# Performance work log

Hardware: AMD Instinct MI355X
Metric: run time of the kernel (lower is better)

Reference implementation:

```python
import jax, jax.numpy as jnp
import numpy as np
from jax import lax

WINDOW_SIZE = 11
SIGMA = 1.5
EPS = 1e-08
C1 = 0.01 ** 2
C2 = 0.03 ** 2


def _gaussian_window(ws, sigma):
    x = jnp.arange(ws, dtype=jnp.float32)
    g = jnp.exp(-((x - ws // 2) ** 2) / (2.0 * sigma ** 2))
    g = g / g.sum()
    w2d = jnp.outer(g, g)  # (ws, ws)
    return w2d[None, None]  # (1,1,ws,ws) OIHW depthwise kernel for C=1


def _normalize(a, b):
    # per-batch min-max normalize, matching torch code exactly
    B = a.shape[0]
    fa = a.reshape(B, -1)
    fb = b.reshape(B, -1)
    mn1 = fa.min(1).reshape(B, 1, 1, 1)
    mx1 = fa.max(1).reshape(B, 1, 1, 1)
    mn2 = fb.min(1).reshape(B, 1, 1, 1)
    mx2 = fb.max(1).reshape(B, 1, 1, 1)
    a = (a - mn1) / (mx1 - mn1 + EPS)
    b = (b - mn2) / (mx2 - mn2 + EPS)
    return a, b


def _dw_conv(x, win):
    # depthwise gaussian blur, SAME-style padding ws//2 (torch conv2d is xcorr;
    # gaussian kernel is symmetric so identical)
    C = x.shape[1]
    k = jnp.broadcast_to(win, (C, 1, WINDOW_SIZE, WINDOW_SIZE))
    pad = WINDOW_SIZE // 2
    return lax.conv_general_dilated(
        x, k, window_strides=(1, 1), padding=[(pad, pad), (pad, pad)],
        feature_group_count=C,
        dimension_numbers=('NCHW', 'OIHW', 'NCHW'))


def _ssim_mean(m1, m2, win):
    mu1 = _dw_conv(m1, win)
    mu2 = _dw_conv(m2, win)
    mu1_sq = mu1 * mu1
    mu2_sq = mu2 * mu2
    mu1_mu2 = mu1 * mu2
    sigma1 = _dw_conv(m1 * m1, win) - mu1_sq
    sigma2 = _dw_conv(m2 * m2, win) - mu2_sq
    sigma12 = _dw_conv(m1 * m2, win) - mu1_mu2
    ssim_map = ((2 * mu1_mu2 + C1) * (2 * sigma12 + C2)) / \
               ((mu1_sq + mu2_sq + C1) * (sigma1 + sigma2 + C2))
    return ssim_map.mean()


def _forward(img1, img2, mask_pos, w):
    B, C, H, W = img1.shape
    cols = mask_pos[:, None] + jnp.arange(w)  # (B, w)
    idx = cols[:, None, None, :]
    s1 = jnp.take_along_axis(img1, idx, axis=3)  # (B,C,H,w)
    s2 = jnp.take_along_axis(img2, idx, axis=3)

    # Faithful to source: normalize is called inside the per-batch loop, so
    # row b is normalized (B-b) times; zero rows stay zero (0/eps).
    def body(carry, b):
        m1, m2 = carry
        m1 = m1.at[b].set(s1[b])
        m2 = m2.at[b].set(s2[b])
        m1, m2 = _normalize(m1, m2)
        return (m1, m2), None

    init = (jnp.zeros_like(s1), jnp.zeros_like(s2))
    (m1, m2), _ = lax.scan(body, init, jnp.arange(B))
    win = _gaussian_window(WINDOW_SIZE, SIGMA)
    return _ssim_mean(m1, m2, win)


def setup_inputs() -> dict:
    key = jax.random.key(0)
    k1, k2, k3 = jax.random.split(key, 3)
    B, Cc, H, W = 8, 1, 1024, 2048
    w = 1024
    img1 = jax.random.uniform(k1, (B, Cc, H, W), dtype=jnp.float32)
    img2 = jax.random.uniform(k2, (B, Cc, H, W), dtype=jnp.float32)
    mask_pos = jax.random.randint(k3, (B,), 0, W - w, dtype=jnp.int64 if jax.config.jax_enable_x64 else jnp.int32)
    return {'img1': img1, 'img2': img2, 'mask_pos': mask_pos, 'mask_width': w}


def reference(img1, img2, mask_pos, mask_width):
    return _forward(img1, img2, mask_pos, int(mask_width))
```

## Files before the change

kernel.cpp:

```cpp
#include <hip/hip_runtime.h>

#define NB 8
#define IMH 1024
#define IMW 2048
#define WM 1024
#define RPB 32
#define CPB 256
#define RBW 272

__device__ __forceinline__ unsigned int enc_f(float f) {
    unsigned int u = __float_as_uint(f);
    return (u & 0x80000000u) ? ~u : (u | 0x80000000u);
}
__device__ __forceinline__ float dec_f(unsigned int u) {
    u = (u & 0x80000000u) ? (u & 0x7fffffffu) : ~u;
    return __uint_as_float(u);
}


__global__ void k_init(unsigned int* ws) {
    int t = threadIdx.x;
    if (t < 16) { ws[t] = 0xFFFFFFFFu; ws[16 + t] = 0u; }
    if (t == 0) *((double*)(ws + 80)) = 0.0;
}

__global__ __launch_bounds__(256) void k_minmax(const float* __restrict__ img1,
                                                const float* __restrict__ img2,
                                                const int* __restrict__ mask_pos,
                                                unsigned int* __restrict__ ws) {
    int bi = blockIdx.x >> 6;
    int img = bi >> 3, b = bi & 7;
    int chunk = blockIdx.x & 63;
    const float* base = (img ? img2 : img1)
        + (size_t)b * IMH * IMW + (size_t)(chunk * 16) * IMW + mask_pos[b];
    int tid = threadIdx.x;
    float mn = 3.4e38f, mx = -3.4e38f;
    for (int idx = tid; idx < 16 * WM; idx += 256) {
        int r = idx >> 10, c = idx & (WM - 1);
        float v = base[(size_t)r * IMW + c];
        mn = fminf(mn, v); mx = fmaxf(mx, v);
    }
    for (int off = 32; off; off >>= 1) {
        mn = fminf(mn, __shfl_down(mn, off));
        mx = fmaxf(mx, __shfl_down(mx, off));
    }
    __shared__ float smn[4], smx[4];
    int lane = tid & 63, wid = tid >> 6;
    if (lane == 0) { smn[wid] = mn; smx[wid] = mx; }
    __syncthreads();
    if (tid == 0) {
        mn = fminf(fminf(smn[0], smn[1]), fminf(smn[2], smn[3]));
        mx = fmaxf(fmaxf(smx[0], smx[1]), fmaxf(smx[2], smx[3]));
        atomicMin(&ws[img * 8 + b], enc_f(mn));
        atomicMax(&ws[16 + img * 8 + b], enc_f(mx));
    }
}

__global__ __launch_bounds__(256) void k_ssim(const float* __restrict__ img1,
                                              const float* __restrict__ img2,
                                              const int* __restrict__ mask_pos,
                                              const unsigned int* __restrict__ ws,
                                              double* __restrict__ acc_g) {
    __shared__ float rb[2][2][RBW];
    __shared__ float red[4];

    const int tid = threadIdx.x;
    const int b  = blockIdx.z;
    const int cb = blockIdx.x * CPB;
    const int r0 = blockIdx.y * RPB;
    const int mp = mask_pos[b];

    float mn1, sc1, mn2, sc2;
    {
        float mnA = dec_f(ws[b]),     mxA = dec_f(ws[16 + b]);
        float mnB = dec_f(ws[8 + b]), mxB = dec_f(ws[24 + b]);
        float rngA = mxA - mnA; float d0A = rngA + 1e-8f; double DA = (double)d0A; float MA = rngA / d0A;
        float rngB = mxB - mnB; float d0B = rngB + 1e-8f; double DB = (double)d0B; float MB = rngB / d0B;
        for (int j = 0; j < 7 - b; ++j) {
            float djA = MA + 1e-8f; DA *= (double)djA; MA = MA / djA;
            float djB = MB + 1e-8f; DB *= (double)djB; MB = MB / djB;
        }
        mn1 = mnA; sc1 = (float)(1.0 / DA);
        mn2 = mnB; sc2 = (float)(1.0 / DB);
    }
    float gw[11];
    {
        float s = 0.f;
#pragma unroll
        for (int k = 0; k < 11; ++k) {
            float x = (float)((k - 5) * (k - 5));
            gw[k] = expf(-x / 4.5f);
            s += gw[k];
        }
#pragma unroll
        for (int k = 0; k < 11; ++k) gw[k] = gw[k] / s;
    }

    const float* b1 = img1 + (size_t)b * (IMH * IMW);
    const float* b2 = img2 + (size_t)b * (IMH * IMW);

    float acc[11][5];
#pragma unroll
    for (int s = 0; s < 11; ++s)
#pragma unroll
        for (int ch = 0; ch < 5; ++ch) acc[s][ch] = 0.f;

    float local = 0.f;

    {
        int rn = r0 - 5;
        float va = 0.f, vb = 0.f, wa = 0.f, wb = 0.f;
        if ((unsigned)rn < (unsigned)IMH) {
            int mcA = cb + tid - 8;
            if ((unsigned)mcA < (unsigned)WM) {
                size_t o = (size_t)rn * IMW + (size_t)(mp + mcA);
                va = (b1[o] - mn1) * sc1; vb = (b2[o] - mn2) * sc2;
            }
            if (tid < RBW - 256) {
                int mcB = cb + 248 + tid;
                if ((unsigned)mcB < (unsigned)WM) {
                    size_t o = (size_t)rn * IMW + (size_t)(mp + mcB);
                    wa = (b1[o] - mn1) * sc1; wb = (b2[o] - mn2) * sc2;
                }
            }
        }
        rb[0][0][tid] = va; rb[0][1][tid] = vb;
        if (tid < RBW - 256) { rb[0][0][256 + tid] = wa; rb[0][1][256 + tid] = wb; }
        __syncthreads();
    }

#pragma unroll 1
    for (int g = 0; g < 4; ++g) {
#pragma unroll
        for (int p = 0; p < 11; ++p) {
            const int i = g * 11 + p;
            const int par = (g + p) & 1;

            int rn = r0 - 4 + i;
            float va = 0.f, vb = 0.f, wa = 0.f, wb = 0.f;
            if ((unsigned)rn < (unsigned)IMH) {
                int mcA = cb + tid - 8;
                if ((unsigned)mcA < (unsigned)WM) {
                    size_t o = (size_t)rn * IMW + (size_t)(mp + mcA);
                    va = (b1[o] - mn1) * sc1; vb = (b2[o] - mn2) * sc2;
                }
                if (tid < RBW - 256) {
                    int mcB = cb + 248 + tid;
                    if ((unsigned)mcB < (unsigned)WM) {
                        size_t o = (size_t)rn * IMW + (size_t)(mp + mcB);
                        wa = (b1[o] - mn1) * sc1; wb = (b2[o] - mn2) * sc2;
                    }
                }
            }

            const float* c0p = &rb[par][0][tid + 3];
            const float* c1p = &rb[par][1][tid + 3];
            float ha = 0.f, hb = 0.f, haa = 0.f, hbb = 0.f, hab = 0.f;
#pragma unroll
            for (int k = 0; k < 11; ++k) {
                float av = c0p[k], bv = c1p[k], w = gw[k];
                ha  = fmaf(w, av, ha);
                hb  = fmaf(w, bv, hb);
                haa = fmaf(w, av * av, haa);
                hbb = fmaf(w, bv * bv, hbb);
                hab = fmaf(w, av * bv, hab);
            }

#pragma unroll
            for (int s = 0; s < 11; ++s) {
                const float w = gw[(p + 10 - s) % 11];
                acc[s][0] = fmaf(w, ha,  acc[s][0]);
                acc[s][1] = fmaf(w, hb,  acc[s][1]);
                acc[s][2] = fmaf(w, haa, acc[s][2]);
                acc[s][3] = fmaf(w, hbb, acc[s][3]);
                acc[s][4] = fmaf(w, hab, acc[s][4]);
            }

            if (i >= 10 && i <= 41) {
                float mu1 = acc[p][0], mu2 = acc[p][1];
                float e11 = acc[p][2], e22 = acc[p][3], e12 = acc[p][4];
                float m11 = mu1 * mu1, m22 = mu2 * mu2, m12 = mu1 * mu2;
                float num = (2.f * m12 + 1e-4f) * (2.f * (e12 - m12) + 9e-4f);
                float den = (m11 + m22 + 1e-4f) * ((e11 - m11) + (e22 - m22) + 9e-4f);
                local += num / den;
            }
            acc[p][0] = 0.f; acc[p][1] = 0.f; acc[p][2] = 0.f;
            acc[p][3] = 0.f; acc[p][4] = 0.f;

            rb[par ^ 1][0][tid] = va; rb[par ^ 1][1][tid] = vb;
            if (tid < RBW - 256) { rb[par ^ 1][0][256 + tid] = wa; rb[par ^ 1][1][256 + tid] = wb; }
            __syncthreads();
        }
    }

    for (int off = 32; off; off >>= 1) local += __shfl_down(local, off);
    int lane = tid & 63, wid = tid >> 6;
    if (lane == 0) red[wid] = local;
    __syncthreads();
    if (tid == 0) {
        double s = (double)red[0] + (double)red[1] + (double)red[2] + (double)red[3];
        atomicAdd(acc_g, s);
    }
}

__global__ void k_final(const double* __restrict__ acc, float* __restrict__ out) {
    out[0] = (float)(acc[0] * (1.0 / 8388608.0));
}

extern "C" void kernel_launch(void* const* d_in, const int* in_sizes, int n_in,
                              void* d_out, int out_size, void* d_ws, size_t ws_size,
                              hipStream_t stream) {
    const float* img1 = (const float*)d_in[0];
    const float* img2 = (const float*)d_in[1];
    const int* mask_pos = (const int*)d_in[2];
    unsigned int* ws = (unsigned int*)d_ws;
    double* acc = (double*)(ws + 80);
    float* out = (float*)d_out;

    hipLaunchKernelGGL(k_init, dim3(1), dim3(64), 0, stream, ws);
    hipLaunchKernelGGL(k_minmax, dim3(1024), dim3(256), 0, stream, img1, img2, mask_pos, ws);
    hipLaunchKernelGGL(k_ssim, dim3(WM / CPB, IMH / RPB, NB), dim3(256), 0, stream,
                       img1, img2, mask_pos, ws, acc);
    hipLaunchKernelGGL(k_final, dim3(1), dim3(1), 0, stream, acc, out);
}
```

Measured before the change: 231.5 us.

## Vectorize minmax loads, interleave SSIM smem buffer, simplify SSIM row loads

The min/max pass now reads with aligned float4 loads and scalar head/tail handling, using twice as many blocks of 8 rows each. The SSIM kernel interleaves the two images in shared memory as float2 pairs and swaps buffers with pointers. Row loads use precomputed offsets and unconditional loads followed by selects. The vertical accumulator reset is folded into a first-write assignment, and the division uses __fdividef. The changes aim to cut memory instruction count and branching, at the cost of more index arithmetic and a slightly less exact division.

```diff
diff --git a/kernel.cpp b/kernel.cpp
--- a/kernel.cpp
+++ b/kernel.cpp
@@ -6,7 +6,6 @@
 #define WM 1024
 #define RPB 32
 #define CPB 256
-#define RBW 272
 
 __device__ __forceinline__ unsigned int enc_f(float f) {
     unsigned int u = __float_as_uint(f);
@@ -28,17 +27,32 @@
                                                 const float* __restrict__ img2,
                                                 const int* __restrict__ mask_pos,
                                                 unsigned int* __restrict__ ws) {
-    int bi = blockIdx.x >> 6;
+    int bi = blockIdx.x >> 7;
     int img = bi >> 3, b = bi & 7;
-    int chunk = blockIdx.x & 63;
+    int rg = blockIdx.x & 127;
     const float* base = (img ? img2 : img1)
-        + (size_t)b * IMH * IMW + (size_t)(chunk * 16) * IMW + mask_pos[b];
+        + (size_t)b * (IMH * IMW) + (size_t)(rg * 8) * IMW + mask_pos[b];
     int tid = threadIdx.x;
     float mn = 3.4e38f, mx = -3.4e38f;
-    for (int idx = tid; idx < 16 * WM; idx += 256) {
-        int r = idx >> 10, c = idx & (WM - 1);
-        float v = base[(size_t)r * IMW + c];
-        mn = fminf(mn, v); mx = fmaxf(mx, v);
+    for (int r = 0; r < 8; ++r) {
+        const float* p = base + (size_t)r * IMW;
+        unsigned mis = ((unsigned)(uintptr_t)p >> 2) & 3u;
+        unsigned s = (4u - mis) & 3u;
+        int nf4 = (int)((1024u - s) >> 2);
+        if (tid < nf4) {
+            float4 v = *(const float4*)(p + s + 4 * tid);
+            mn = fminf(mn, fminf(fminf(v.x, v.y), fminf(v.z, v.w)));
+            mx = fmaxf(mx, fmaxf(fmaxf(v.x, v.y), fmaxf(v.z, v.w)));
+        }
+        if (tid >= 248) {
+            unsigned e = tid - 248;
+            unsigned rem0 = s + 4u * (unsigned)nf4;
+            unsigned tc = 1024u - rem0;
+            unsigned idx = 0; bool ok = false;
+            if (e < s) { idx = e; ok = true; }
+            else if (e >= 4u && (e - 4u) < tc) { idx = rem0 + (e - 4u); ok = true; }
+            if (ok) { float v = p[idx]; mn = fminf(mn, v); mx = fmaxf(mx, v); }
+        }
     }
     for (int off = 32; off; off >>= 1) {
         mn = fminf(mn, __shfl_down(mn, off));
@@ -61,7 +75,7 @@
                                               const int* __restrict__ mask_pos,
                                               const unsigned int* __restrict__ ws,
                                               double* __restrict__ acc_g) {
-    __shared__ float rb[2][2][RBW];
+    __shared__ float rb[2][1024];
     __shared__ float red[4];
 
     const int tid = threadIdx.x;
@@ -96,71 +110,68 @@
         for (int k = 0; k < 11; ++k) gw[k] = gw[k] / s;
     }
 
-    const float* b1 = img1 + (size_t)b * (IMH * IMW);
-    const float* b2 = img2 + (size_t)b * (IMH * IMW);
+    const float* bs1 = img1 + (size_t)b * (IMH * IMW) + (ptrdiff_t)(r0 - 5) * IMW + mp;
+    const float* bs2 = img2 + (size_t)b * (IMH * IMW) + (ptrdiff_t)(r0 - 5) * IMW + mp;
+
+    const int mcA = cb + tid - 8;
+    const bool okA = (unsigned)mcA < (unsigned)WM;
+    const int mcB = cb + 248 + tid;
+    const bool okB = (tid < 16) && ((unsigned)mcB < (unsigned)WM);
+    unsigned voffA = (unsigned)(okA ? mcA : 0);
+    unsigned voffB = (unsigned)(((unsigned)mcB < (unsigned)WM) ? mcB : 0);
 
     float acc[11][5];
 #pragma unroll
     for (int s = 0; s < 11; ++s)
 #pragma unroll
         for (int ch = 0; ch < 5; ++ch) acc[s][ch] = 0.f;
-
     float local = 0.f;
 
+    const float* cur = &rb[0][0];
+    float* nxt;
+
     {
-        int rn = r0 - 5;
         float va = 0.f, vb = 0.f, wa = 0.f, wb = 0.f;
-        if ((unsigned)rn < (unsigned)IMH) {
-            int mcA = cb + tid - 8;
-            if ((unsigned)mcA < (unsigned)WM) {
-                size_t o = (size_t)rn * IMW + (size_t)(mp + mcA);
-                va = (b1[o] - mn1) * sc1; vb = (b2[o] - mn2) * sc2;
-            }
-            if (tid < RBW - 256) {
-                int mcB = cb + 248 + tid;
-                if ((unsigned)mcB < (unsigned)WM) {
-                    size_t o = (size_t)rn * IMW + (size_t)(mp + mcB);
-                    wa = (b1[o] - mn1) * sc1; wb = (b2[o] - mn2) * sc2;
-                }
-            }
-        }
-        rb[0][0][tid] = va; rb[0][1][tid] = vb;
-        if (tid < RBW - 256) { rb[0][0][256 + tid] = wa; rb[0][1][256 + tid] = wb; }
+        if ((unsigned)(r0 - 5) < (unsigned)IMH) {
+            float x1 = bs1[voffA], x2 = bs2[voffA];
+            float y1 = bs1[voffB], y2 = bs2[voffB];
+            va = okA ? (x1 - mn1) * sc1 : 0.f;
+            vb = okA ? (x2 - mn2) * sc2 : 0.f;
+            wa = okB ? (y1 - mn1) * sc1 : 0.f;
+            wb = okB ? (y2 - mn2) * sc2 : 0.f;
+        }
+        voffA += IMW; voffB += IMW;
+        float* w0 = (float*)&rb[0][0];
+        *(float2*)&w0[2 * tid] = make_float2(va, vb);
+        *(float2*)&w0[2 * (256 + tid)] = make_float2(wa, wb);
         __syncthreads();
     }
+    nxt = (float*)&rb[1][0];
 
 #pragma unroll 1
     for (int g = 0; g < 4; ++g) {
 #pragma unroll
         for (int p = 0; p < 11; ++p) {
             const int i = g * 11 + p;
-            const int par = (g + p) & 1;
-
-            int rn = r0 - 4 + i;
+
             float va = 0.f, vb = 0.f, wa = 0.f, wb = 0.f;
-            if ((unsigned)rn < (unsigned)IMH) {
-                int mcA = cb + tid - 8;
-                if ((unsigned)mcA < (unsigned)WM) {
-                    size_t o = (size_t)rn * IMW + (size_t)(mp + mcA);
-                    va = (b1[o] - mn1) * sc1; vb = (b2[o] - mn2) * sc2;
-                }
-                if (tid < RBW - 256) {
-                    int mcB = cb + 248 + tid;
-                    if ((unsigned)mcB < (unsigned)WM) {
-                        size_t o = (size_t)rn * IMW + (size_t)(mp + mcB);
-                        wa = (b1[o] - mn1) * sc1; wb = (b2[o] - mn2) * sc2;
-                    }
-                }
-            }
-
-            const float* c0p = &rb[par][0][tid + 3];
-            const float* c1p = &rb[par][1][tid + 3];
-            float ha = 0.f, hb = 0.f, haa = 0.f, hbb = 0.f, hab = 0.f;
+            if ((unsigned)(r0 - 4 + i) < (unsigned)IMH) {
+                float x1 = bs1[voffA], x2 = bs2[voffA];
+                float y1 = bs1[voffB], y2 = bs2[voffB];
+                va = okA ? (x1 - mn1) * sc1 : 0.f;
+                vb = okA ? (x2 - mn2) * sc2 : 0.f;
+                wa = okB ? (y1 - mn1) * sc1 : 0.f;
+                wb = okB ? (y2 - mn2) * sc2 : 0.f;
+            }
+            voffA += IMW; voffB += IMW;
+
+            float ha = 0.f, hbv = 0.f, haa = 0.f, hbb = 0.f, hab = 0.f;
 #pragma unroll
             for (int k = 0; k < 11; ++k) {
-                float av = c0p[k], bv = c1p[k], w = gw[k];
+                float2 e = *(const float2*)&cur[2 * (tid + 3 + k)];
+                float av = e.x, bv = e.y, w = gw[k];
                 ha  = fmaf(w, av, ha);
-                hb  = fmaf(w, bv, hb);
+                hbv = fmaf(w, bv, hbv);
                 haa = fmaf(w, av * av, haa);
                 hbb = fmaf(w, bv * bv, hbb);
                 hab = fmaf(w, av * bv, hab);
@@ -169,11 +180,16 @@
 #pragma unroll
             for (int s = 0; s < 11; ++s) {
                 const float w = gw[(p + 10 - s) % 11];
-                acc[s][0] = fmaf(w, ha,  acc[s][0]);
-                acc[s][1] = fmaf(w, hb,  acc[s][1]);
-                acc[s][2] = fmaf(w, haa, acc[s][2]);
-                acc[s][3] = fmaf(w, hbb, acc[s][3]);
-                acc[s][4] = fmaf(w, hab, acc[s][4]);
+                if (s == (p + 10) % 11) {
+                    acc[s][0] = w * ha;  acc[s][1] = w * hbv; acc[s][2] = w * haa;
+                    acc[s][3] = w * hbb; acc[s][4] = w * hab;
+                } else {
+                    acc[s][0] = fmaf(w, ha,  acc[s][0]);
+                    acc[s][1] = fmaf(w, hbv, acc[s][1]);
+                    acc[s][2] = fmaf(w, haa, acc[s][2]);
+                    acc[s][3] = fmaf(w, hbb, acc[s][3]);
+                    acc[s][4] = fmaf(w, hab, acc[s][4]);
+                }
             }
 
             if (i >= 10 && i <= 41) {
@@ -182,14 +198,13 @@
                 float m11 = mu1 * mu1, m22 = mu2 * mu2, m12 = mu1 * mu2;
                 float num = (2.f * m12 + 1e-4f) * (2.f * (e12 - m12) + 9e-4f);
                 float den = (m11 + m22 + 1e-4f) * ((e11 - m11) + (e22 - m22) + 9e-4f);
-                local += num / den;
-            }
-            acc[p][0] = 0.f; acc[p][1] = 0.f; acc[p][2] = 0.f;
-            acc[p][3] = 0.f; acc[p][4] = 0.f;
-
-            rb[par ^ 1][0][tid] = va; rb[par ^ 1][1][tid] = vb;
-            if (tid < RBW - 256) { rb[par ^ 1][0][256 + tid] = wa; rb[par ^ 1][1][256 + tid] = wb; }
+                local += __fdividef(num, den);
+            }
+
+            *(float2*)&nxt[2 * tid] = make_float2(va, vb);
+            *(float2*)&nxt[2 * (256 + tid)] = make_float2(wa, wb);
             __syncthreads();
+            { const float* t = cur; cur = nxt; nxt = (float*)t; }
         }
     }
 
@@ -218,7 +233,7 @@
     float* out = (float*)d_out;
 
     hipLaunchKernelGGL(k_init, dim3(1), dim3(64), 0, stream, ws);
-    hipLaunchKernelGGL(k_minmax, dim3(1024), dim3(256), 0, stream, img1, img2, mask_pos, ws);
+    hipLaunchKernelGGL(k_minmax, dim3(2048), dim3(256), 0, stream, img1, img2, mask_pos, ws);
     hipLaunchKernelGGL(k_ssim, dim3(WM / CPB, IMH / RPB, NB), dim3(256), 0, stream,
                        img1, img2, mask_pos, ws, acc);
     hipLaunchKernelGGL(k_final, dim3(1), dim3(1), 0, stream, acc, out);
```

Result: faster. 218.2 us (-5.7%).
